# Optimization experiments

Hardware: AMD Instinct MI355X
Metric: run time of the kernel (lower is better)

Reference implementation:

```python
import jax, jax.numpy as jnp
import numpy as np

N_E = 1024
E_DIM = 256
TAU = 0.5
BETA = 0.25
LAMB = 0.1
EPS = 1e-10


def setup_inputs() -> dict:
    key = jax.random.key(0)
    k1, k2, k3 = jax.random.split(key, 3)
    z = jax.random.normal(k1, (16, 1024, E_DIM), dtype=jnp.float32)
    # kaiming-normal-initialized codebook (std = sqrt(2 / fan_in))
    emb = jax.random.normal(k2, (N_E, E_DIM), dtype=jnp.float32) * np.sqrt(2.0 / E_DIM)
    u = jax.random.uniform(k3, (16 * 1024, N_E), dtype=jnp.float32)
    return {"z": z, "emb": emb, "u": u}


def reference(z, emb, u):
    zf = z.reshape(-1, E_DIM)                                  # [N, e_dim]
    # squared euclidean distances to each code: ||z||^2 + ||e||^2 - 2 z.e
    d = (jnp.sum(zf * zf, axis=1, keepdims=True)
         + jnp.sum(emb * emb, axis=1)
         - 2.0 * jnp.matmul(zf, emb.T))                        # [N, n_e]
    # gumbel-softmax (hard, straight-through) on logits = -d
    g = -jnp.log(-jnp.log(u + EPS) + EPS)
    y_soft = jax.nn.softmax((-d + g) / TAU, axis=-1)
    idx = jnp.argmax(y_soft, axis=-1)
    y_hard = jax.nn.one_hot(idx, N_E, dtype=y_soft.dtype)
    probs = y_hard + y_soft - jax.lax.stop_gradient(y_soft)    # [N, n_e]
    z_q = jnp.matmul(probs, emb).reshape(z.shape)
    # orthogonality loss on the codebook gram matrix
    gram = jnp.matmul(emb, emb.T)
    ortho = jnp.mean((gram - jnp.eye(N_E, dtype=emb.dtype)) ** 2) / (N_E ** 2)
    emb_loss = jnp.mean((jax.lax.stop_gradient(z_q) - z) ** 2)
    commit = BETA * jnp.mean((z_q - jax.lax.stop_gradient(z)) ** 2)
    loss = emb_loss + BETA * commit + LAMB * ortho
    z_q_st = z + jax.lax.stop_gradient(z_q - z)
    e_mean = jnp.mean(probs, axis=0)
    perplexity = jnp.exp(-jnp.sum(e_mean * jnp.log(e_mean + EPS)))
    return loss, z_q_st, perplexity
```

## Files before the change

kernel.cpp:

```cpp
#include <hip/hip_runtime.h>
#include <math.h>
#include <stdint.h>


#define NROWS 16384
#define NE    1024
#define ED    256
#define EPSF  1e-10f
#define INV2048 4.8828125e-4f
#define BM 64
#define BN 64

typedef _Float16 half_t;
typedef __attribute__((ext_vector_type(4))) _Float16 half4;
typedef __attribute__((ext_vector_type(8))) _Float16 half8;
typedef __attribute__((ext_vector_type(16))) float floatx16;
typedef unsigned long long u64;

__device__ __forceinline__ void gl_lds16(const void* g, void* l) {
    __builtin_amdgcn_global_load_lds(
        (const __attribute__((address_space(1))) uint32_t*)g,
        (__attribute__((address_space(3))) uint32_t*)l, 16, 0, 0);
}

__device__ __forceinline__ u64 packMax(float v, int code) {
    unsigned int b   = __float_as_uint(v);
    unsigned int key = (b & 0x80000000u) ? ~b : (b | 0x80000000u);
    return ((u64)key << 32) | (unsigned int)(NE - 1 - code);
}

__global__ __launch_bounds__(256) void vq_prep(
        const float* __restrict__ z, const float* __restrict__ emb,
        half_t* __restrict__ zh, half_t* __restrict__ zl,
        half_t* __restrict__ eh, half_t* __restrict__ el,
        float* __restrict__ enorm, float* __restrict__ znorm,
        u64* __restrict__ best)
{
    const int gid = blockIdx.x * 256 + threadIdx.x;
    const int ZQ8 = NROWS * ED / 8;
    if (gid < ZQ8) {
        const float4 v0 = ((const float4*)z)[(size_t)gid * 2];
        const float4 v1 = ((const float4*)z)[(size_t)gid * 2 + 1];
        const float x[8] = {v0.x, v0.y, v0.z, v0.w, v1.x, v1.y, v1.z, v1.w};
        half8 h, l;
        float s = 0.f;
#pragma unroll
        for (int i = 0; i < 8; ++i) {
            const half_t hi = (half_t)x[i];
            h[i] = hi; l[i] = (half_t)((x[i] - (float)hi) * 2048.0f);
            s = fmaf(x[i], x[i], s);
        }
        *(half8*)&zh[(size_t)gid * 8] = h;
        *(half8*)&zl[(size_t)gid * 8] = l;
#pragma unroll
        for (int o = 16; o; o >>= 1) s += __shfl_down(s, o, 32);
        if ((threadIdx.x & 31) == 0) znorm[gid >> 5] = s;
    } else {
        const int eg = gid - ZQ8;
        const float4 v0 = ((const float4*)emb)[(size_t)eg * 2];
        const float4 v1 = ((const float4*)emb)[(size_t)eg * 2 + 1];
        const float x[8] = {v0.x, v0.y, v0.z, v0.w, v1.x, v1.y, v1.z, v1.w};
        half8 h, l;
        float s = 0.f;
#pragma unroll
        for (int i = 0; i < 8; ++i) {
            const half_t hi = (half_t)x[i];
            h[i] = hi; l[i] = (half_t)((x[i] - (float)hi) * 2048.0f);
            s = fmaf(x[i], x[i], s);
        }
        *(half8*)&eh[(size_t)eg * 8] = h;
        *(half8*)&el[(size_t)eg * 8] = l;
#pragma unroll
        for (int o = 16; o; o >>= 1) s += __shfl_down(s, o, 32);
        if ((threadIdx.x & 31) == 0) enorm[eg >> 5] = s;
        if (eg < NROWS) best[eg] = 0ull;
    }
}

__global__ __launch_bounds__(256, 4) void vq_gemm(
        const half_t* __restrict__ zh, const half_t* __restrict__ zl,
        const half_t* __restrict__ eh, const half_t* __restrict__ el,
        const float* __restrict__ u, const float* __restrict__ enorm,
        u64* __restrict__ best)
{
    __shared__ __align__(16) char smem[32768];
    half_t* Ch = (half_t*)smem;
    half_t* Cl = (half_t*)(smem + 8192);
    half_t* Zh = (half_t*)(smem + 16384);
    half_t* Zl = (half_t*)(smem + 24576);
    u64* parr = (u64*)smem;

    const int t    = threadIdx.x;
    const int w    = t >> 6;
    const int lane = t & 63;
    const int lrow = lane & 31;
    const int hw   = lane >> 5;

    const int bid = blockIdx.x;
    const int xcd = bid & 7, c = bid >> 3;
    const int m0 = (xcd * 32 + (c >> 4)) * BM;
    const int n0 = (c & 15) * BN;
    const int wr = w >> 1, wc = w & 1;

    size_t gcoff[2], gzoff[2];
#pragma unroll
    for (int it = 0; it < 2; ++it) {
        const int s = it * 256 + t;
        const int row = s >> 3;
        const int cc = (s & 7) ^ (row & 7);
        gcoff[it] = (size_t)(n0 + row) * ED + cc * 8;
        gzoff[it] = (size_t)(m0 + row) * ED + cc * 8;
    }

    auto STAGE = [&](int kc) {
#pragma unroll
        for (int it = 0; it < 2; ++it) {
            const int ldso = (it * 256 + w * 64) * 8;
            gl_lds16(eh + gcoff[it] + kc, Ch + ldso);
            gl_lds16(el + gcoff[it] + kc, Cl + ldso);
            gl_lds16(zh + gzoff[it] + kc, Zh + ldso);
            gl_lds16(zl + gzoff[it] + kc, Zl + ldso);
        }
    };

    const int myrow = m0 + wr * 32 + lrow;
    const int cbase = n0 + wc * 32 + (hw << 2);
    float4 uf[4];
    {
        const float* up = u + (size_t)myrow * NE + cbase;
        uf[0] = *(const float4*)(up);
        uf[1] = *(const float4*)(up + 8);
        uf[2] = *(const float4*)(up + 16);
        uf[3] = *(const float4*)(up + 24);
    }

    floatx16 accH = {};
    floatx16 accX = {};

    STAGE(0);
    for (int kc = 0; kc < ED; kc += 64) {
        __syncthreads();
#pragma unroll
        for (int ks = 0; ks < 4; ++ks) {
            const int cch = ks * 2 + hw;
            const int cr = wc * 32 + lrow;
            const int zr = wr * 32 + lrow;
            const int sc_ = cr * 8 + (cch ^ (cr & 7));
            const int sz_ = zr * 8 + (cch ^ (zr & 7));
            const half8 ch8 = *(const half8*)&Ch[sc_ * 8];
            const half8 cl8 = *(const half8*)&Cl[sc_ * 8];
            const half8 zh8 = *(const half8*)&Zh[sz_ * 8];
            const half8 zl8 = *(const half8*)&Zl[sz_ * 8];
            accH = __builtin_amdgcn_mfma_f32_32x32x16_f16(ch8, zh8, accH, 0, 0, 0);
            accX = __builtin_amdgcn_mfma_f32_32x32x16_f16(ch8, zl8, accX, 0, 0, 0);
            accX = __builtin_amdgcn_mfma_f32_32x32x16_f16(cl8, zh8, accX, 0, 0, 0);
        }
        if (kc == 0) {
#pragma unroll
            for (int q = 0; q < 4; ++q)
                asm volatile("" :: "v"(uf[q].x), "v"(uf[q].y),
                                   "v"(uf[q].z), "v"(uf[q].w));
        }
        __syncthreads();
        if (kc + 64 < ED) STAGE(kc + 64);
    }

    float4 ef[4];
    {
        const float* ep = enorm + cbase;
        ef[0] = *(const float4*)(ep);
        ef[1] = *(const float4*)(ep + 8);
        ef[2] = *(const float4*)(ep + 16);
        ef[3] = *(const float4*)(ep + 24);
    }
    u64 bestp = 0ull;
#pragma unroll
    for (int r = 0; r < 16; ++r) {
        const int q = r >> 2, j = r & 3;
        const float uv = ((const float*)&uf[q])[j];
        const float en = ((const float*)&ef[q])[j];
        const float d  = accH[r] + accX[r] * INV2048;
        const float g  = -__logf(-__logf(uv + EPSF) + EPSF);
        const float sc = 2.f * d - en + g;
        const u64 pm = packMax(sc, cbase + j + (q << 3));
        if (pm > bestp) bestp = pm;
    }
    {
        const unsigned int lo = (unsigned int)bestp;
        const unsigned int hi = (unsigned int)(bestp >> 32);
        const unsigned int lo2 = __shfl_down(lo, 32);
        const unsigned int hi2 = __shfl_down(hi, 32);
        const u64 o = ((u64)hi2 << 32) | lo2;
        if (o > bestp) bestp = o;
    }
    if (lrow == lane) {
        parr[(wr * 32 + lrow) * 2 + wc] = bestp;
    }
    __syncthreads();
    if (t < 64) {
        const u64 a = parr[t * 2], b = parr[t * 2 + 1];
        atomicMax(&best[m0 + t], a > b ? a : b);
    }
}

__global__ __launch_bounds__(256) void vq_outstore(
        const float* __restrict__ emb, const u64* __restrict__ best,
        const float* __restrict__ znorm, const float* __restrict__ u,
        int* __restrict__ idxArr, double* __restrict__ partial,
        float* __restrict__ out)
{
    __shared__ int   ridx[8];
    __shared__ float rmse[8];
    const int t  = threadIdx.x;
    const int m0 = blockIdx.x * 8;

    if (t < 8) {
        const u64 p = best[m0 + t];
        const unsigned int key = (unsigned int)(p >> 32);
        const int code = NE - 1 - (int)(p & 0xFFFFFFFFu);
        ridx[t] = code;
        idxArr[m0 + t] = code;
        const unsigned int b = (key & 0x80000000u) ? (key ^ 0x80000000u) : ~key;
        const float s  = __uint_as_float(b);
        const float uv = u[(size_t)(m0 + t) * NE + code];
        const float g  = -__logf(-__logf(uv + EPSF) + EPSF);
        rmse[t] = znorm[m0 + t] - s + g;
    }
    __syncthreads();
    if (t == 0) {
        double acc = 0.0;
#pragma unroll
        for (int r = 0; r < 8; ++r) acc += (double)rmse[r];
        partial[blockIdx.x] = acc;
    }

#pragma unroll
    for (int rr = 0; rr < 8; ++rr) {
        const int j = ridx[rr];
        out[1 + (size_t)(m0 + rr) * ED + t] = emb[(size_t)j * ED + t];
    }
}

__global__ __launch_bounds__(256) void vq_fin(
        const int* __restrict__ idxArr, const double* __restrict__ partial,
        float* __restrict__ out)
{
    __shared__ int    hist[NE];
    __shared__ double redl[4], redp[4];
    const int t = threadIdx.x;

    for (int i = t; i < NE; i += 256) hist[i] = 0;
    __syncthreads();

    for (int r = t; r < NROWS; r += 256)
        atomicAdd(&hist[idxArr[r]], 1);

    double lsum = 0.0;
    for (int b = t; b < NROWS / 8; b += 256)
        lsum += partial[b];
    __syncthreads();

    double psum = 0.0;
    for (int i = t; i < NE; i += 256) {
        const float em = (float)hist[i] / (float)NROWS;
        psum += (double)(em * logf(em + EPSF));
    }

#pragma unroll
    for (int o = 32; o; o >>= 1) { lsum += __shfl_down(lsum, o); psum += __shfl_down(psum, o); }
    if ((t & 63) == 0) { redl[t >> 6] = lsum; redp[t >> 6] = psum; }
    __syncthreads();
    if (t == 0) {
        const double mse = (redl[0] + redl[1] + redl[2] + redl[3])
                           / (double)((size_t)NROWS * ED);
        const double tot = redp[0] + redp[1] + redp[2] + redp[3];
        out[0] = (float)(mse * 1.0625);
        out[1 + (size_t)NROWS * ED] = (float)exp(-tot);
    }
}

extern "C" void kernel_launch(void* const* d_in, const int* in_sizes, int n_in,
                              void* d_out, int out_size, void* d_ws, size_t ws_size,
                              hipStream_t stream) {
    const float* z   = (const float*)d_in[0];
    const float* emb = (const float*)d_in[1];
    const float* u   = (const float*)d_in[2];
    float* out = (float*)d_out;

    float*  enorm    = (float*)((char*)d_ws + 5120);
    u64*    best     = (u64*)((char*)d_ws + 9216);
    float*  znorm    = (float*)((char*)d_ws + 140288);
    int*    idxArr   = (int*)((char*)d_ws + 205824);
    double* partial  = (double*)((char*)d_ws + 271360);
    const size_t small_end = 287744;

    const size_t zsplit = (size_t)NROWS * ED * 2;
    const size_t esplit = (size_t)NE * ED * 2;
    const bool bigws = ws_size >= small_end + 2 * zsplit + 2 * esplit;

    half_t *zh, *zl, *eh, *el;
    if (bigws) {
        char* big = (char*)d_ws + small_end;
        zh = (half_t*)big;
        zl = (half_t*)(big + zsplit);
        eh = (half_t*)(big + 2 * zsplit);
        el = (half_t*)(big + 2 * zsplit + esplit);
    } else {
        zh = (half_t*)((char*)d_out + 8);
        zl = (half_t*)((char*)d_out + 8 + zsplit);
        eh = (half_t*)((char*)d_ws + small_end);
        el = (half_t*)((char*)d_ws + small_end + esplit);
    }

    vq_prep<<<(NROWS * ED / 8 + NE * ED / 8) / 256, 256, 0, stream>>>(
        z, emb, zh, zl, eh, el, enorm, znorm, best);
    vq_gemm<<<(NROWS / BM) * (NE / BN), 256, 0, stream>>>(
        zh, zl, eh, el, u, enorm, best);
    vq_outstore<<<NROWS / 8, 256, 0, stream>>>(
        emb, best, znorm, u, idxArr, partial, out);
    vq_fin<<<1, 256, 0, stream>>>(idxArr, partial, out);
}
```

Before: 176.0 us.

## Fuse argmax finalize into a row-panel GEMM that sweeps the full codebook

The GEMM is restructured so each 512-thread block owns 64 rows and walks all 1024 codes in 8 panels. The block keeps its z-high fragments in registers, double-buffers the codebook tiles in LDS and prefetches the next panel's u values. Because each block now sees every code, the global u64 atomicMax buffer and its zero-initialisation go away, and the per-row argmax decode and loss partial are computed in the GEMM epilogue. The separate outstore and final-reduction kernels are merged into one launch. In exchange the grid shrinks from 4096 to 256 large blocks using about 100KB of LDS each, which lowers occupancy and latency hiding.

Measured after the change: 167.5 us. -4.9%, faster.

```diff
diff --git a/kernel.cpp b/kernel.cpp
--- a/kernel.cpp
+++ b/kernel.cpp
@@ -8,8 +8,9 @@
 #define ED    256
 #define EPSF  1e-10f
 #define INV2048 4.8828125e-4f
-#define BM 64
-#define BN 64
+#define BMF 64
+#define PW  128
+#define NPAN 8
 
 typedef _Float16 half_t;
 typedef __attribute__((ext_vector_type(4))) _Float16 half4;
@@ -33,8 +34,7 @@
         const float* __restrict__ z, const float* __restrict__ emb,
         half_t* __restrict__ zh, half_t* __restrict__ zl,
         half_t* __restrict__ eh, half_t* __restrict__ el,
-        float* __restrict__ enorm, float* __restrict__ znorm,
-        u64* __restrict__ best)
+        float* __restrict__ enorm, float* __restrict__ znorm)
 {
     const int gid = blockIdx.x * 256 + threadIdx.x;
     const int ZQ8 = NROWS * ED / 8;
@@ -73,118 +73,154 @@
 #pragma unroll
         for (int o = 16; o; o >>= 1) s += __shfl_down(s, o, 32);
         if ((threadIdx.x & 31) == 0) enorm[eg >> 5] = s;
-        if (eg < NROWS) best[eg] = 0ull;
-    }
-}
-
-__global__ __launch_bounds__(256, 4) void vq_gemm(
+    }
+}
+
+__global__ __launch_bounds__(512, 2) void vq_gemmf(
         const half_t* __restrict__ zh, const half_t* __restrict__ zl,
         const half_t* __restrict__ eh, const half_t* __restrict__ el,
         const float* __restrict__ u, const float* __restrict__ enorm,
-        u64* __restrict__ best)
+        const float* __restrict__ znorm,
+        int* __restrict__ idxArr, double* __restrict__ partial)
 {
-    __shared__ __align__(16) char smem[32768];
-    half_t* Ch = (half_t*)smem;
-    half_t* Cl = (half_t*)(smem + 8192);
-    half_t* Zh = (half_t*)(smem + 16384);
-    half_t* Zl = (half_t*)(smem + 24576);
-    u64* parr = (u64*)smem;
+    __shared__ __align__(16) char smem[100352];
+    half_t* SH  = (half_t*)smem;
+    half_t* ZlH = (half_t*)(smem + 65536);
+    u64*   parr = (u64*)(smem + 98304);
 
     const int t    = threadIdx.x;
     const int w    = t >> 6;
     const int lane = t & 63;
     const int lrow = lane & 31;
     const int hw   = lane >> 5;
-
-    const int bid = blockIdx.x;
-    const int xcd = bid & 7, c = bid >> 3;
-    const int m0 = (xcd * 32 + (c >> 4)) * BM;
-    const int n0 = (c & 15) * BN;
-    const int wr = w >> 1, wc = w & 1;
-
-    size_t gcoff[2], gzoff[2];
+    const int wr   = w >> 2, wcq = w & 3;
+
+    const int m0    = blockIdx.x * BMF;
+    const int rl    = wr * 32 + lrow;
+    const int myrow = m0 + rl;
+
+    size_t zOff[4];
+#pragma unroll
+    for (int it = 0; it < 4; ++it) {
+        const int s = it * 512 + t;
+        const int row = s >> 5;
+        const int ch = (s & 31) ^ (row & 31);
+        zOff[it] = (size_t)(m0 + row) * ED + ch * 8;
+    }
+    size_t bOff[2];
 #pragma unroll
     for (int it = 0; it < 2; ++it) {
-        const int s = it * 256 + t;
+        const int s = it * 512 + t;
         const int row = s >> 3;
-        const int cc = (s & 7) ^ (row & 7);
-        gcoff[it] = (size_t)(n0 + row) * ED + cc * 8;
-        gzoff[it] = (size_t)(m0 + row) * ED + cc * 8;
-    }
-
-    auto STAGE = [&](int kc) {
+        const int ch = (s & 7) ^ (row & 7);
+        bOff[it] = (size_t)row * ED + ch * 8;
+    }
+
+    auto STAGE_B = [&](int pb, int kcA, int bufI) {
+        half_t* d0 = SH + bufI * 16384;
+        const size_t add = (size_t)pb * ED + kcA * 64;
 #pragma unroll
         for (int it = 0; it < 2; ++it) {
-            const int ldso = (it * 256 + w * 64) * 8;
-            gl_lds16(eh + gcoff[it] + kc, Ch + ldso);
-            gl_lds16(el + gcoff[it] + kc, Cl + ldso);
-            gl_lds16(zh + gzoff[it] + kc, Zh + ldso);
-            gl_lds16(zl + gzoff[it] + kc, Zl + ldso);
+            const int ldso = (it * 512 + w * 64) * 8;
+            gl_lds16(eh + bOff[it] + add, d0 + ldso);
+            gl_lds16(el + bOff[it] + add, d0 + 8192 + ldso);
         }
     };
 
-    const int myrow = m0 + wr * 32 + lrow;
-    const int cbase = n0 + wc * 32 + (hw << 2);
-    float4 uf[4];
+#pragma unroll
+    for (int it = 0; it < 4; ++it) {
+        const int ldso = (it * 512 + w * 64) * 8;
+        gl_lds16(zh + zOff[it], SH + ldso);
+        gl_lds16(zl + zOff[it], ZlH + ldso);
+    }
+    float4 ufC[4], ufN[4];
     {
-        const float* up = u + (size_t)myrow * NE + cbase;
-        uf[0] = *(const float4*)(up);
-        uf[1] = *(const float4*)(up + 8);
-        uf[2] = *(const float4*)(up + 16);
-        uf[3] = *(const float4*)(up + 24);
-    }
+        const float* up = u + (size_t)myrow * NE + wcq * 32 + (hw << 2);
+        ufC[0] = *(const float4*)(up);
+        ufC[1] = *(const float4*)(up + 8);
+        ufC[2] = *(const float4*)(up + 16);
+        ufC[3] = *(const float4*)(up + 24);
+    }
+    __syncthreads();
+
+    half8 zf[16];
+#pragma unroll
+    for (int f = 0; f < 16; ++f) {
+        const int chz = 2 * f + hw;
+        const int sz = rl * 32 + (chz ^ (rl & 31));
+        zf[f] = *(const half8*)&SH[sz * 8];
+    }
+    __syncthreads();
+    STAGE_B(0, 0, 0);
 
     floatx16 accH = {};
     floatx16 accX = {};
-
-    STAGE(0);
-    for (int kc = 0; kc < ED; kc += 64) {
-        __syncthreads();
-#pragma unroll
-        for (int ks = 0; ks < 4; ++ks) {
-            const int cch = ks * 2 + hw;
-            const int cr = wc * 32 + lrow;
-            const int zr = wr * 32 + lrow;
-            const int sc_ = cr * 8 + (cch ^ (cr & 7));
-            const int sz_ = zr * 8 + (cch ^ (zr & 7));
-            const half8 ch8 = *(const half8*)&Ch[sc_ * 8];
-            const half8 cl8 = *(const half8*)&Cl[sc_ * 8];
-            const half8 zh8 = *(const half8*)&Zh[sz_ * 8];
-            const half8 zl8 = *(const half8*)&Zl[sz_ * 8];
-            accH = __builtin_amdgcn_mfma_f32_32x32x16_f16(ch8, zh8, accH, 0, 0, 0);
-            accX = __builtin_amdgcn_mfma_f32_32x32x16_f16(ch8, zl8, accX, 0, 0, 0);
-            accX = __builtin_amdgcn_mfma_f32_32x32x16_f16(cl8, zh8, accX, 0, 0, 0);
-        }
-        if (kc == 0) {
-#pragma unroll
-            for (int q = 0; q < 4; ++q)
-                asm volatile("" :: "v"(uf[q].x), "v"(uf[q].y),
-                                   "v"(uf[q].z), "v"(uf[q].w));
-        }
-        __syncthreads();
-        if (kc + 64 < ED) STAGE(kc + 64);
-    }
-
-    float4 ef[4];
-    {
-        const float* ep = enorm + cbase;
-        ef[0] = *(const float4*)(ep);
-        ef[1] = *(const float4*)(ep + 8);
-        ef[2] = *(const float4*)(ep + 16);
-        ef[3] = *(const float4*)(ep + 24);
-    }
     u64 bestp = 0ull;
-#pragma unroll
-    for (int r = 0; r < 16; ++r) {
-        const int q = r >> 2, j = r & 3;
-        const float uv = ((const float*)&uf[q])[j];
-        const float en = ((const float*)&ef[q])[j];
-        const float d  = accH[r] + accX[r] * INV2048;
-        const float g  = -__logf(-__logf(uv + EPSF) + EPSF);
-        const float sc = 2.f * d - en + g;
-        const u64 pm = packMax(sc, cbase + j + (q << 3));
-        if (pm > bestp) bestp = pm;
-    }
+
+    for (int p = 0; p < NPAN; ++p) {
+        const int pbase = p * PW;
+#pragma unroll
+        for (int kc = 0; kc < 4; ++kc) {
+            __syncthreads();
+            if (kc == 0 && p < NPAN - 1) {
+                const float* up = u + (size_t)myrow * NE + pbase + PW
+                                    + wcq * 32 + (hw << 2);
+                ufN[0] = *(const float4*)(up);
+                ufN[1] = *(const float4*)(up + 8);
+                ufN[2] = *(const float4*)(up + 16);
+                ufN[3] = *(const float4*)(up + 24);
+            }
+            if (kc < 3)                STAGE_B(pbase, kc + 1, (kc & 1) ^ 1);
+            else if (p < NPAN - 1)     STAGE_B(pbase + PW, 0, (kc & 1) ^ 1);
+            half_t* cb = SH + (kc & 1) * 16384;
+#pragma unroll
+            for (int ks = 0; ks < 4; ++ks) {
+                const int f = kc * 4 + ks;
+                const int cchL = ks * 2 + hw;
+                const int crow = wcq * 32 + lrow;
+                const int sb = crow * 8 + (cchL ^ (crow & 7));
+                const half8 ch8 = *(const half8*)&cb[sb * 8];
+                const half8 cl8 = *(const half8*)&cb[8192 + sb * 8];
+                const int chz = 2 * f + hw;
+                const int szz = rl * 32 + (chz ^ (rl & 31));
+                const half8 zl8 = *(const half8*)&ZlH[szz * 8];
+                accH = __builtin_amdgcn_mfma_f32_32x32x16_f16(ch8, zf[f], accH, 0, 0, 0);
+                accX = __builtin_amdgcn_mfma_f32_32x32x16_f16(ch8, zl8, accX, 0, 0, 0);
+                accX = __builtin_amdgcn_mfma_f32_32x32x16_f16(cl8, zf[f], accX, 0, 0, 0);
+            }
+            if (kc == 1 && p < NPAN - 1) {
+#pragma unroll
+                for (int q = 0; q < 4; ++q)
+                    asm volatile("" :: "v"(ufN[q].x), "v"(ufN[q].y),
+                                       "v"(ufN[q].z), "v"(ufN[q].w));
+            }
+        }
+        const int cbase = pbase + wcq * 32 + (hw << 2);
+        float4 ef[4];
+        {
+            const float* ep = enorm + cbase;
+            ef[0] = *(const float4*)(ep);
+            ef[1] = *(const float4*)(ep + 8);
+            ef[2] = *(const float4*)(ep + 16);
+            ef[3] = *(const float4*)(ep + 24);
+        }
+#pragma unroll
+        for (int r = 0; r < 16; ++r) {
+            const int q = r >> 2, j = r & 3;
+            const float uv = ((const float*)&ufC[q])[j];
+            const float en = ((const float*)&ef[q])[j];
+            const float d  = accH[r] + accX[r] * INV2048;
+            const float g  = -__logf(-__logf(uv + EPSF) + EPSF);
+            const float sc = 2.f * d - en + g;
+            const u64 pm = packMax(sc, cbase + j + (q << 3));
+            if (pm > bestp) bestp = pm;
+        }
+        accH = (floatx16){};
+        accX = (floatx16){};
+#pragma unroll
+        for (int q = 0; q < 4; ++q) ufC[q] = ufN[q];
+    }
+
     {
         const unsigned int lo = (unsigned int)bestp;
         const unsigned int hi = (unsigned int)(bestp >> 32);
@@ -193,89 +229,71 @@
         const u64 o = ((u64)hi2 << 32) | lo2;
         if (o > bestp) bestp = o;
     }
-    if (lrow == lane) {
-        parr[(wr * 32 + lrow) * 2 + wc] = bestp;
-    }
+    if (hw == 0) parr[rl * 4 + wcq] = bestp;
     __syncthreads();
+
     if (t < 64) {
-        const u64 a = parr[t * 2], b = parr[t * 2 + 1];
-        atomicMax(&best[m0 + t], a > b ? a : b);
-    }
-}
-
-__global__ __launch_bounds__(256) void vq_outstore(
-        const float* __restrict__ emb, const u64* __restrict__ best,
-        const float* __restrict__ znorm, const float* __restrict__ u,
-        int* __restrict__ idxArr, double* __restrict__ partial,
-        float* __restrict__ out)
-{
-    __shared__ int   ridx[8];
-    __shared__ float rmse[8];
-    const int t  = threadIdx.x;
-    const int m0 = blockIdx.x * 8;
-
-    if (t < 8) {
-        const u64 p = best[m0 + t];
+        const u64 b0 = parr[t * 4],     b1 = parr[t * 4 + 1];
+        const u64 b2 = parr[t * 4 + 2], b3 = parr[t * 4 + 3];
+        const u64 m1 = b0 > b1 ? b0 : b1;
+        const u64 m2 = b2 > b3 ? b2 : b3;
+        const u64 p  = m1 > m2 ? m1 : m2;
         const unsigned int key = (unsigned int)(p >> 32);
         const int code = NE - 1 - (int)(p & 0xFFFFFFFFu);
-        ridx[t] = code;
         idxArr[m0 + t] = code;
         const unsigned int b = (key & 0x80000000u) ? (key ^ 0x80000000u) : ~key;
         const float s  = __uint_as_float(b);
         const float uv = u[(size_t)(m0 + t) * NE + code];
         const float g  = -__logf(-__logf(uv + EPSF) + EPSF);
-        rmse[t] = znorm[m0 + t] - s + g;
-    }
+        float lm = znorm[m0 + t] - s + g;
+#pragma unroll
+        for (int o = 32; o; o >>= 1) lm += __shfl_down(lm, o);
+        if (t == 0) partial[blockIdx.x] = (double)lm;
+    }
+}
+
+__global__ __launch_bounds__(256) void vq_out(
+        const float* __restrict__ emb, const int* __restrict__ idxArr,
+        const double* __restrict__ partial, float* __restrict__ out)
+{
+    const int t = threadIdx.x;
+
+    if (blockIdx.x == NROWS / 8) {
+        __shared__ int    hist[NE];
+        __shared__ double redl[4], redp[4];
+        for (int i = t; i < NE; i += 256) hist[i] = 0;
+        __syncthreads();
+        for (int r = t; r < NROWS; r += 256)
+            atomicAdd(&hist[idxArr[r]], 1);
+        double lsum = (t < NROWS / BMF) ? partial[t] : 0.0;
+        __syncthreads();
+        double psum = 0.0;
+        for (int i = t; i < NE; i += 256) {
+            const float em = (float)hist[i] / (float)NROWS;
+            psum += (double)(em * logf(em + EPSF));
+        }
+#pragma unroll
+        for (int o = 32; o; o >>= 1) { lsum += __shfl_down(lsum, o); psum += __shfl_down(psum, o); }
+        if ((t & 63) == 0) { redl[t >> 6] = lsum; redp[t >> 6] = psum; }
+        __syncthreads();
+        if (t == 0) {
+            const double mse = (redl[0] + redl[1] + redl[2] + redl[3])
+                               / (double)((size_t)NROWS * ED);
+            const double tot = redp[0] + redp[1] + redp[2] + redp[3];
+            out[0] = (float)(mse * 1.0625);
+            out[1 + (size_t)NROWS * ED] = (float)exp(-tot);
+        }
+        return;
+    }
+
+    __shared__ int ridx[8];
+    const int m0 = blockIdx.x * 8;
+    if (t < 8) ridx[t] = idxArr[m0 + t];
     __syncthreads();
-    if (t == 0) {
-        double acc = 0.0;
-#pragma unroll
-        for (int r = 0; r < 8; ++r) acc += (double)rmse[r];
-        partial[blockIdx.x] = acc;
-    }
-
 #pragma unroll
     for (int rr = 0; rr < 8; ++rr) {
         const int j = ridx[rr];
         out[1 + (size_t)(m0 + rr) * ED + t] = emb[(size_t)j * ED + t];
-    }
-}
-
-__global__ __launch_bounds__(256) void vq_fin(
-        const int* __restrict__ idxArr, const double* __restrict__ partial,
-        float* __restrict__ out)
-{
-    __shared__ int    hist[NE];
-    __shared__ double redl[4], redp[4];
-    const int t = threadIdx.x;
-
-    for (int i = t; i < NE; i += 256) hist[i] = 0;
-    __syncthreads();
-
-    for (int r = t; r < NROWS; r += 256)
-        atomicAdd(&hist[idxArr[r]], 1);
-
-    double lsum = 0.0;
-    for (int b = t; b < NROWS / 8; b += 256)
-        lsum += partial[b];
-    __syncthreads();
-
-    double psum = 0.0;
-    for (int i = t; i < NE; i += 256) {
-        const float em = (float)hist[i] / (float)NROWS;
-        psum += (double)(em * logf(em + EPSF));
-    }
-
-#pragma unroll
-    for (int o = 32; o; o >>= 1) { lsum += __shfl_down(lsum, o); psum += __shfl_down(psum, o); }
-    if ((t & 63) == 0) { redl[t >> 6] = lsum; redp[t >> 6] = psum; }
-    __syncthreads();
-    if (t == 0) {
-        const double mse = (redl[0] + redl[1] + redl[2] + redl[3])
-                           / (double)((size_t)NROWS * ED);
-        const double tot = redp[0] + redp[1] + redp[2] + redp[3];
-        out[0] = (float)(mse * 1.0625);
-        out[1 + (size_t)NROWS * ED] = (float)exp(-tot);
     }
 }
 
@@ -287,12 +305,11 @@
     const float* u   = (const float*)d_in[2];
     float* out = (float*)d_out;
 
-    float*  enorm    = (float*)((char*)d_ws + 5120);
-    u64*    best     = (u64*)((char*)d_ws + 9216);
-    float*  znorm    = (float*)((char*)d_ws + 140288);
-    int*    idxArr   = (int*)((char*)d_ws + 205824);
-    double* partial  = (double*)((char*)d_ws + 271360);
-    const size_t small_end = 287744;
+    float*  enorm   = (float*)((char*)d_ws + 4096);
+    float*  znorm   = (float*)((char*)d_ws + 8192);
+    int*    idxArr  = (int*)((char*)d_ws + 73728);
+    double* partial = (double*)((char*)d_ws + 139264);
+    const size_t small_end = 141312;
 
     const size_t zsplit = (size_t)NROWS * ED * 2;
     const size_t esplit = (size_t)NE * ED * 2;
@@ -313,10 +330,8 @@
     }
 
     vq_prep<<<(NROWS * ED / 8 + NE * ED / 8) / 256, 256, 0, stream>>>(
-        z, emb, zh, zl, eh, el, enorm, znorm, best);
-    vq_gemm<<<(NROWS / BM) * (NE / BN), 256, 0, stream>>>(
-        zh, zl, eh, el, u, enorm, best);
-    vq_outstore<<<NROWS / 8, 256, 0, stream>>>(
-        emb, best, znorm, u, idxArr, partial, out);
-    vq_fin<<<1, 256, 0, stream>>>(idxArr, partial, out);
-}
+        z, emb, zh, zl, eh, el, enorm, znorm);
+    vq_gemmf<<<NROWS / BMF, 512, 0, stream>>>(
+        zh, zl, eh, el, u, enorm, znorm, idxArr, partial);
+    vq_out<<<NROWS / 8 + 1, 256, 0, stream>>>(emb, idxArr, partial, out);
+}
```
